# Kernel optimization log

Measured on AMD Instinct MI355X. Metric: run time of the kernel, lower is better.

Reference implementation:

```python
import jax, jax.numpy as jnp
import numpy as np

H = 8          # SD1.4 heads
TAU = 0.1      # HarmCfg.tau
GAMMA = 1.0    # HarmCfg.gamma
EPS = 1e-12    # F.normalize eps


def setup_inputs() -> dict:
    key = jax.random.key(0)
    ks = jax.random.split(key, 8)
    B, S, C, K, D = 16, 4096, 320, 77, 768
    return {
        "hidden_states": jax.random.normal(ks[0], (B, S, C), jnp.float32),
        "encoder_hidden_states": jax.random.normal(ks[1], (B, K, D), jnp.float32),
        "harm_vec": jax.random.normal(ks[2], (D,), jnp.float32),
        "Wq": jax.random.normal(ks[3], (C, C), jnp.float32) * 0.02,
        "Wk": jax.random.normal(ks[4], (D, C), jnp.float32) * 0.02,
        "Wv": jax.random.normal(ks[5], (D, C), jnp.float32) * 0.02,
        "Wo": jax.random.normal(ks[6], (C, C), jnp.float32) * 0.02,
        "bo": jnp.zeros((C,), jnp.float32),
    }


def reference(hidden_states, encoder_hidden_states, harm_vec, Wq, Wk, Wv, Wo, bo):
    B, S, C = hidden_states.shape
    K = encoder_hidden_states.shape[1]
    dh = C // H
    scale = 1.0 / jnp.sqrt(jnp.asarray(dh, hidden_states.dtype))

    # projections (no bias on q/k/v, as in diffusers SD1.4)
    q = (hidden_states @ Wq).reshape(B, S, H, dh)
    k = (encoder_hidden_states @ Wk).reshape(B, K, H, dh)
    v = (encoder_hidden_states @ Wv).reshape(B, K, H, dh)

    # scores: QK^T / sqrt(dh)  -> [B, H, S, K]
    scores = jnp.einsum('bqhd,bkhd->bhqk', q, k) * scale

    # cosine-similarity harmful-token penalty (broadcast over heads and queries)
    harm = harm_vec / jnp.maximum(jnp.linalg.norm(harm_vec), EPS)
    ctx_norm = encoder_hidden_states / jnp.maximum(
        jnp.linalg.norm(encoder_hidden_states, axis=-1, keepdims=True), EPS)
    cos = jnp.einsum('bkd,d->bk', ctx_norm, harm)            # [B, K]
    penalty = jnp.maximum(cos - TAU, 0.0)                     # clamp(min=0)
    scores = scores - GAMMA * penalty[:, None, None, :]

    probs = jax.nn.softmax(scores, axis=-1)                   # dropout p=0 (eval)
    out = jnp.einsum('bhqk,bkhd->bqhd', probs, v).reshape(B, S, C)
    return out @ Wo + bo
```

## Files before the change

### kernel.cpp

```cpp
#include <hip/hip_runtime.h>
#include <hip/hip_bf16.h>

#define B_ 16
#define S_ 4096
#define C_ 320
#define KK_ 77
#define D_ 768
#define H_ 8
#define DH_ 40
#define KP_ 80
#define NP_ (H_ * KP_)
#define TAU_ 0.1f
#define GAMMA_ 1.0f
#define EPS_ 1e-12f

typedef __bf16 bf16x8 __attribute__((ext_vector_type(8)));
typedef float f32x4 __attribute__((ext_vector_type(4)));
typedef unsigned short ushort8v __attribute__((ext_vector_type(8)));
typedef unsigned int u32;

#define WAITV(N)  asm volatile("s_waitcnt vmcnt(" #N ")" ::: "memory")
#define WAITLG()  asm volatile("s_waitcnt lgkmcnt(0)" ::: "memory")
#define BAR()     __builtin_amdgcn_s_barrier()

__device__ __forceinline__ unsigned short f2bf(float f) {
    union { float f; unsigned u; } v; v.f = f;
    unsigned r = v.u + 0x7fffu + ((v.u >> 16) & 1u);
    return (unsigned short)(r >> 16);
}

__device__ __forceinline__ void gld16(const unsigned short* g, char* l) {
    __builtin_amdgcn_global_load_lds(
        (const __attribute__((address_space(1))) u32*)g,
        (__attribute__((address_space(3))) u32*)l, 16, 0, 0);
}

__global__ __launch_bounds__(256) void build_M(const float* __restrict__ Wq,
        const float* __restrict__ Wk, const float* __restrict__ Wv,
        const float* __restrict__ Wo, unsigned short* __restrict__ Bmat) {
    const int Dk = blockIdx.x * 256 + threadIdx.x;
    const int h = blockIdx.y;
    const int which = blockIdx.z >> 2;
    const int c0 = (blockIdx.z & 3) * 80;
    __shared__ float wlds[80 * 44];
    for (int i = threadIdx.x; i < 80 * DH_; i += 256) {
        int c = i / DH_, d = i % DH_;
        wlds[c * 44 + d] = which
            ? Wo[(size_t)(h * DH_ + d) * C_ + (c0 + c)]
            : Wq[(size_t)(c0 + c) * C_ + h * DH_ + d];
    }
    float a[DH_];
    const float* Arow = (which ? Wv : Wk) + (size_t)Dk * C_ + h * DH_;
    #pragma unroll
    for (int d = 0; d < DH_; ++d) a[d] = Arow[d];
    __syncthreads();
    const float scale = 0.15811388300841898f;
    for (int c = 0; c < 80; ++c) {
        float s = 0.f;
        #pragma unroll
        for (int q = 0; q < 10; ++q) {
            float4 wv4 = *(const float4*)&wlds[c * 44 + q * 4];
            s += a[q * 4 + 0] * wv4.x + a[q * 4 + 1] * wv4.y
               + a[q * 4 + 2] * wv4.z + a[q * 4 + 3] * wv4.w;
        }
        if (!which) s *= scale;
        int n = which * 2560 + h * C_ + c0 + c;
        Bmat[(size_t)n * D_ + Dk] = f2bf(s);
    }
}

__global__ __launch_bounds__(256) void prep_ehs(const float* __restrict__ ehs,
        const float* __restrict__ harm, unsigned short* __restrict__ ehs_bf,
        float* __restrict__ pen) {
    const int w = threadIdx.x >> 6, l = threadIdx.x & 63;
    const int kk = blockIdx.x * 4 + w, b = blockIdx.y;
    const size_t obase = ((size_t)b * KP_ + kk) * D_;
    if (kk >= KK_) {
        #pragma unroll
        for (int j = 0; j < 12; ++j) ehs_bf[obase + l + j * 64] = 0;
        if (l == 0) pen[b * KP_ + kk] = 0.f;
        return;
    }
    const float* er = ehs + ((size_t)b * KK_ + kk) * D_;
    float ss = 0.f, dd = 0.f, hh = 0.f;
    #pragma unroll
    for (int j = 0; j < 12; ++j) {
        float e = er[l + j * 64], hv = harm[l + j * 64];
        ehs_bf[obase + l + j * 64] = f2bf(e);
        ss += e * e; dd += e * hv; hh += hv * hv;
    }
    #pragma unroll
    for (int off = 32; off; off >>= 1) {
        ss += __shfl_xor(ss, off);
        dd += __shfl_xor(dd, off);
        hh += __shfl_xor(hh, off);
    }
    if (l == 0) {
        float cs = dd / (fmaxf(sqrtf(ss), EPS_) * fmaxf(sqrtf(hh), EPS_));
        pen[b * KP_ + kk] = GAMMA_ * fmaxf(cs - TAU_, 0.f);
    }
}

__global__ __launch_bounds__(1024) void gemm_WpU(
        const unsigned short* __restrict__ ehs_bf,
        const unsigned short* __restrict__ Bmat,
        unsigned short* __restrict__ Wp, unsigned short* __restrict__ U) {
    const int id = blockIdx.x;
    const int b = id & 15, nt = id >> 4;
    const int tid = threadIdx.x, w = tid >> 6, l = tid & 63;
    const int lrow = l & 15, lgrp = l >> 4, lk = lgrp * 8;
    __shared__ unsigned short Al[80 * 768];
    char* lds = (char*)Al;

    const unsigned short* Ag = ehs_bf + (size_t)b * KP_ * D_;
    #pragma unroll
    for (int it = 0; it < 8; ++it) {
        int ch = tid + it * 1024;
        if (ch < 7680) {
            int byte = ch * 16, row = byte / 1536;
            int a = byte ^ ((row & 7) << 4);
            *(ushort8v*)(lds + a) = *(const ushort8v*)(Ag + ch * 8);
        }
    }
    const int n0 = nt * 512 + w * 32;
    const unsigned short* Br = Bmat + (size_t)(n0 + lrow) * D_ + lk;
    bf16x8 bC[2], bN[2];
    #pragma unroll
    for (int nf = 0; nf < 2; ++nf)
        bC[nf] = *(const bf16x8*)(Br + (size_t)nf * 16 * D_);
    __syncthreads();

    f32x4 acc[5][2];
    #pragma unroll
    for (int mf = 0; mf < 5; ++mf)
        #pragma unroll
        for (int nf = 0; nf < 2; ++nf) acc[mf][nf] = (f32x4){0.f, 0.f, 0.f, 0.f};
    #pragma unroll
    for (int ks = 0; ks < D_ / 32; ++ks) {
        if (ks < D_ / 32 - 1) {
            #pragma unroll
            for (int nf = 0; nf < 2; ++nf)
                bN[nf] = *(const bf16x8*)(Br + (size_t)nf * 16 * D_ + (ks + 1) * 32);
        }
        bf16x8 af[5];
        #pragma unroll
        for (int mf = 0; mf < 5; ++mf) {
            int row = mf * 16 + lrow;
            int a = (row * 1536 + (ks * 32 + lk) * 2) ^ ((row & 7) << 4);
            af[mf] = *(const bf16x8*)(lds + a);
        }
        __builtin_amdgcn_s_setprio(1);
        #pragma unroll
        for (int mf = 0; mf < 5; ++mf)
            #pragma unroll
            for (int nf = 0; nf < 2; ++nf)
                acc[mf][nf] = __builtin_amdgcn_mfma_f32_16x16x32_bf16(
                    af[mf], bC[nf], acc[mf][nf], 0, 0, 0);
        __builtin_amdgcn_s_setprio(0);
        #pragma unroll
        for (int nf = 0; nf < 2; ++nf) bC[nf] = bN[nf];
    }
    #pragma unroll
    for (int nf = 0; nf < 2; ++nf) {
        const int col = n0 + nf * 16 + lrow;
        if (col < 2560) {
            const int h = col / C_, c = col % C_;
            #pragma unroll
            for (int mf = 0; mf < 5; ++mf)
                #pragma unroll
                for (int r = 0; r < 4; ++r) {
                    int kk = mf * 16 + lgrp * 4 + r;
                    Wp[((size_t)b * NP_ + h * KP_ + kk) * C_ + c] = f2bf(acc[mf][nf][r]);
                }
        } else {
            const int n2 = col - 2560;
            const int h = n2 / C_, c = n2 % C_;
            #pragma unroll
            for (int mf = 0; mf < 5; ++mf)
                #pragma unroll
                for (int r = 0; r < 4; ++r) {
                    int kk = mf * 16 + lgrp * 4 + r;
                    U[((size_t)b * C_ + c) * NP_ + h * KP_ + kk] = f2bf(acc[mf][nf][r]);
                }
        }
    }
}

__global__ __launch_bounds__(512, 2) void fused_attn(
        const float* __restrict__ hs, const unsigned short* __restrict__ Wp,
        const unsigned short* __restrict__ U, const float* __restrict__ pen,
        const float* __restrict__ bo, float* __restrict__ out) {
    const int id = blockIdx.x;
    const int xcd = id & 7, rest = id >> 3;
    const int b = xcd * 2 + (rest >> 6);
    const int s0 = (rest & 63) * 64;
    __shared__ __align__(16) char smem[163840];
    char* HS = smem;
    char* PB = smem;
    const int tid = threadIdx.x, w = tid >> 6, l = tid & 63;
    const int lrow = l & 15, lgrp = l >> 4, lk = lgrp * 8;
    const int h = w;
    const int mgrp = w & 1, ngrp = w >> 1;
    char* wbuf = smem + 40960 + w * 3 * 5120;
    char* ubuf = smem + 81920 + w * 2 * 5120;

    const unsigned short* Wpb = Wp + ((size_t)b * NP_ + h * KP_) * C_;
    const unsigned short* Ub  = U  + ((size_t)b * C_ + ngrp * 80) * NP_;

    auto stage_wp = [&](int ks, int slot) {
        char* buf = wbuf + slot * 5120;
        #pragma unroll
        for (int j = 0; j < 5; ++j) {
            int L = j * 64 + l;
            int n = L >> 2, cs = (L & 3) ^ (n & 3);
            gld16(Wpb + (size_t)n * C_ + ks * 32 + cs * 8, buf + j * 1024);
        }
    };
    auto stage_u = [&](int t, int slot) {
        char* buf = ubuf + slot * 5120;
        #pragma unroll
        for (int j = 0; j < 5; ++j) {
            int L = j * 64 + l;
            int c = L >> 2, cs = (L & 3) ^ (c & 3);
            gld16(Ub + (size_t)c * NP_ + t * 32 + cs * 8, buf + j * 1024);
        }
    };

    float4 pv4[5];
    #pragma unroll
    for (int nf = 0; nf < 5; ++nf)
        pv4[nf] = *(const float4*)(pen + b * KP_ + nf * 16 + lgrp * 4);
    const float4* hv = (const float4*)(hs + ((size_t)b * S_ + s0) * C_);
    #pragma unroll
    for (int it = 0; it < 10; ++it) {
        int i = tid + it * 512;
        float4 v = hv[i];
        int r = i / 80, c = (i * 4) % C_;
        ushort4 u;
        u.x = f2bf(v.x); u.y = f2bf(v.y); u.z = f2bf(v.z); u.w = f2bf(v.w);
        int a = (r * 640 + c * 2) ^ ((r & 7) << 4);
        *(ushort4*)(HS + a) = u;
    }
    __syncthreads();
    stage_wp(0, 0);
    stage_wp(1, 1);
    stage_wp(2, 2);

    f32x4 acc[5][4];
    #pragma unroll
    for (int nf = 0; nf < 5; ++nf)
        #pragma unroll
        for (int mf = 0; mf < 4; ++mf) acc[nf][mf] = (f32x4){0.f, 0.f, 0.f, 0.f};
    #pragma unroll
    for (int ks = 0; ks < 10; ++ks) {
        if (ks <= 7)      { WAITV(10); }
        else if (ks == 8) { WAITV(5); }
        else              { WAITV(0); }
        char* rb = wbuf + (ks % 3) * 5120;
        bf16x8 bC[5], hf[4];
        #pragma unroll
        for (int nf = 0; nf < 5; ++nf) {
            int n = nf * 16 + lrow;
            bC[nf] = *(const bf16x8*)(rb + n * 64 + ((lgrp ^ (n & 3)) << 4));
        }
        #pragma unroll
        for (int mf = 0; mf < 4; ++mf) {
            int row = mf * 16 + lrow;
            int a = (row * 640 + (ks * 32 + lk) * 2) ^ ((row & 7) << 4);
            hf[mf] = *(const bf16x8*)(HS + a);
        }
        WAITLG();
        if (ks < 7) stage_wp(ks + 3, ks % 3);
        __builtin_amdgcn_s_setprio(1);
        #pragma unroll
        for (int nf = 0; nf < 5; ++nf)
            #pragma unroll
            for (int mf = 0; mf < 4; ++mf)
                acc[nf][mf] = __builtin_amdgcn_mfma_f32_16x16x32_bf16(
                    bC[nf], hf[mf], acc[nf][mf], 0, 0, 0);
        __builtin_amdgcn_s_setprio(0);
    }

    float inv4[4];
    #pragma unroll
    for (int mf = 0; mf < 4; ++mf) {
        float mx = -1e30f;
        #pragma unroll
        for (int nf = 0; nf < 5; ++nf)
            #pragma unroll
            for (int r = 0; r < 4; ++r) {
                float x = acc[nf][mf][r] - ((const float*)&pv4[nf])[r];
                if (nf == 4 && r >= 1) x = (lgrp == 3) ? -1e30f : x;
                acc[nf][mf][r] = x;
                mx = fmaxf(mx, x);
            }
        mx = fmaxf(mx, __shfl_xor(mx, 16));
        mx = fmaxf(mx, __shfl_xor(mx, 32));
        float s = 0.f;
        #pragma unroll
        for (int nf = 0; nf < 5; ++nf)
            #pragma unroll
            for (int r = 0; r < 4; ++r) {
                float e = __expf(acc[nf][mf][r] - mx);
                acc[nf][mf][r] = e; s += e;
            }
        s += __shfl_xor(s, 16);
        s += __shfl_xor(s, 32);
        inv4[mf] = 1.f / s;
    }

    BAR();

    #pragma unroll
    for (int mf = 0; mf < 4; ++mf) {
        const int m = mf * 16 + lrow;
        const float inv = inv4[mf];
        #pragma unroll
        for (int nf = 0; nf < 5; ++nf) {
            ushort4 u;
            u.x = f2bf(acc[nf][mf][0] * inv);
            u.y = f2bf(acc[nf][mf][1] * inv);
            u.z = f2bf(acc[nf][mf][2] * inv);
            u.w = f2bf(acc[nf][mf][3] * inv);
            int a = (m * 1280 + (h * KP_ + nf * 16 + lgrp * 4) * 2) ^ ((m & 7) << 4);
            *(ushort4*)(PB + a) = u;
        }
    }
    stage_u(0, 0);
    stage_u(1, 1);
    WAITLG();
    BAR();

    f32x4 acc2[5][2];
    #pragma unroll
    for (int nf = 0; nf < 5; ++nf)
        #pragma unroll
        for (int mf = 0; mf < 2; ++mf) acc2[nf][mf] = (f32x4){0.f, 0.f, 0.f, 0.f};
    #pragma unroll
    for (int t = 0; t < 20; ++t) {
        if (t <= 18) { WAITV(5); } else { WAITV(0); }
        char* rb = ubuf + (t & 1) * 5120;
        bf16x8 pa[2], uf[5];
        #pragma unroll
        for (int mf = 0; mf < 2; ++mf) {
            int m = mgrp * 32 + mf * 16 + lrow;
            int a = (m * 1280 + (t * 32 + lk) * 2) ^ ((m & 7) << 4);
            pa[mf] = *(const bf16x8*)(PB + a);
        }
        #pragma unroll
        for (int nf = 0; nf < 5; ++nf) {
            int c = nf * 16 + lrow;
            uf[nf] = *(const bf16x8*)(rb + c * 64 + ((lgrp ^ (c & 3)) << 4));
        }
        WAITLG();
        if (t < 18) stage_u(t + 2, t & 1);
        __builtin_amdgcn_s_setprio(1);
        #pragma unroll
        for (int nf = 0; nf < 5; ++nf)
            #pragma unroll
            for (int mf = 0; mf < 2; ++mf)
                acc2[nf][mf] = __builtin_amdgcn_mfma_f32_16x16x32_bf16(
                    pa[mf], uf[nf], acc2[nf][mf], 0, 0, 0);
        __builtin_amdgcn_s_setprio(0);
    }

    float bov[5];
    #pragma unroll
    for (int nf = 0; nf < 5; ++nf) bov[nf] = bo[ngrp * 80 + nf * 16 + lrow];
    float* op = out + ((size_t)b * S_ + s0) * C_;
    #pragma unroll
    for (int mf = 0; mf < 2; ++mf)
        #pragma unroll
        for (int r = 0; r < 4; ++r)
            #pragma unroll
            for (int nf = 0; nf < 5; ++nf)
                op[(size_t)(mgrp * 32 + mf * 16 + lgrp * 4 + r) * C_ +
                   ngrp * 80 + nf * 16 + lrow] = acc2[nf][mf][r] + bov[nf];
}

extern "C" void kernel_launch(void* const* d_in, const int* in_sizes, int n_in,
                              void* d_out, int out_size, void* d_ws, size_t ws_size,
                              hipStream_t stream) {
    const float* hs   = (const float*)d_in[0];
    const float* ehs  = (const float*)d_in[1];
    const float* harm = (const float*)d_in[2];
    const float* Wq   = (const float*)d_in[3];
    const float* Wk   = (const float*)d_in[4];
    const float* Wv   = (const float*)d_in[5];
    const float* Wo   = (const float*)d_in[6];
    const float* bo   = (const float*)d_in[7];
    float* out = (float*)d_out;

    char* ws = (char*)d_ws;
    unsigned short* ehs_bf = (unsigned short*)(ws);
    unsigned short* Bmat   = (unsigned short*)(ws + 1966080);
    float*          pen    = (float*)        (ws + 9830400);
    unsigned short* Wp     = (unsigned short*)(ws + 9835520);
    unsigned short* U      = (unsigned short*)(ws + 16389120);

    build_M <<<dim3(3, 8, 8),  256, 0, stream>>>(Wq, Wk, Wv, Wo, Bmat);
    prep_ehs<<<dim3(20, 16),   256, 0, stream>>>(ehs, harm, ehs_bf, pen);
    gemm_WpU<<<dim3(160),     1024, 0, stream>>>(ehs_bf, Bmat, Wp, U);
    fused_attn<<<dim3(1024),   512, 0, stream>>>(hs, Wp, U, pen, bo, out);
}
```

Measured before the change: 167.0 us.

## Share LDS staging across waves with 64-wide k-steps and block barriers

Replaces per-wave private triple- and double-buffered staging of Wp and U tiles with one block-wide shared buffer that all waves fill cooperatively. Each k-step is doubled to 64, so there are fewer pipeline iterations, and the buffers use an 8-way XOR swizzle. U prefetch now starts before the softmax so it overlaps with it. The cost is an added block barrier per step and shallower prefetch: Wp is now single-buffered with a full vmcnt(0) wait each step, which can expose global-load latency.

```diff
diff --git a/kernel.cpp b/kernel.cpp
--- a/kernel.cpp
+++ b/kernel.cpp
@@ -20,6 +20,7 @@
 typedef unsigned int u32;
 
 #define WAITV(N)  asm volatile("s_waitcnt vmcnt(" #N ")" ::: "memory")
+#define WAITVL(N) asm volatile("s_waitcnt vmcnt(" #N ") lgkmcnt(0)" ::: "memory")
 #define WAITLG()  asm volatile("s_waitcnt lgkmcnt(0)" ::: "memory")
 #define BAR()     __builtin_amdgcn_s_barrier()
 
@@ -196,33 +197,34 @@
     const int s0 = (rest & 63) * 64;
     __shared__ __align__(16) char smem[163840];
     char* HS = smem;
+    char* WB = smem + 40960;
     char* PB = smem;
+    char* U0 = smem + 81920;
+    char* U1 = smem + 122880;
     const int tid = threadIdx.x, w = tid >> 6, l = tid & 63;
     const int lrow = l & 15, lgrp = l >> 4, lk = lgrp * 8;
     const int h = w;
     const int mgrp = w & 1, ngrp = w >> 1;
-    char* wbuf = smem + 40960 + w * 3 * 5120;
-    char* ubuf = smem + 81920 + w * 2 * 5120;
-
-    const unsigned short* Wpb = Wp + ((size_t)b * NP_ + h * KP_) * C_;
-    const unsigned short* Ub  = U  + ((size_t)b * C_ + ngrp * 80) * NP_;
-
-    auto stage_wp = [&](int ks, int slot) {
-        char* buf = wbuf + slot * 5120;
+
+    const unsigned short* Wpb = Wp + ((size_t)b * NP_) * C_;
+    const unsigned short* Ub  = U  + ((size_t)b * C_) * NP_;
+
+    auto stage_wp = [&](int s) {
+        #pragma unroll
+        for (int j = 0; j < 10; ++j) {
+            int ch = w * 640 + j * 64 + l;
+            int n = ch >> 3, q = ch & 7;
+            gld16(Wpb + (size_t)n * C_ + s * 64 + ((q ^ (n & 7)) << 3),
+                  WB + ch * 16);
+        }
+    };
+    auto stage_u = [&](int t, char* buf) {
         #pragma unroll
         for (int j = 0; j < 5; ++j) {
-            int L = j * 64 + l;
-            int n = L >> 2, cs = (L & 3) ^ (n & 3);
-            gld16(Wpb + (size_t)n * C_ + ks * 32 + cs * 8, buf + j * 1024);
-        }
-    };
-    auto stage_u = [&](int t, int slot) {
-        char* buf = ubuf + slot * 5120;
-        #pragma unroll
-        for (int j = 0; j < 5; ++j) {
-            int L = j * 64 + l;
-            int c = L >> 2, cs = (L & 3) ^ (c & 3);
-            gld16(Ub + (size_t)c * NP_ + t * 32 + cs * 8, buf + j * 1024);
+            int ch = w * 320 + j * 64 + l;
+            int c = ch >> 3, q = ch & 7;
+            gld16(Ub + (size_t)c * NP_ + t * 64 + ((q ^ (c & 7)) << 3),
+                  buf + ch * 16);
         }
     };
 
@@ -242,9 +244,7 @@
         *(ushort4*)(HS + a) = u;
     }
     __syncthreads();
-    stage_wp(0, 0);
-    stage_wp(1, 1);
-    stage_wp(2, 2);
+    stage_wp(0);
 
     f32x4 acc[5][4];
     #pragma unroll
@@ -252,34 +252,45 @@
         #pragma unroll
         for (int mf = 0; mf < 4; ++mf) acc[nf][mf] = (f32x4){0.f, 0.f, 0.f, 0.f};
     #pragma unroll
-    for (int ks = 0; ks < 10; ++ks) {
-        if (ks <= 7)      { WAITV(10); }
-        else if (ks == 8) { WAITV(5); }
-        else              { WAITV(0); }
-        char* rb = wbuf + (ks % 3) * 5120;
-        bf16x8 bC[5], hf[4];
+    for (int s = 0; s < 5; ++s) {
+        WAITV(0);
+        BAR();
+        bf16x8 bC[5][2], hf[4][2];
         #pragma unroll
         for (int nf = 0; nf < 5; ++nf) {
-            int n = nf * 16 + lrow;
-            bC[nf] = *(const bf16x8*)(rb + n * 64 + ((lgrp ^ (n & 3)) << 4));
+            int n = h * KP_ + nf * 16 + lrow;
+            #pragma unroll
+            for (int ss = 0; ss < 2; ++ss)
+                bC[nf][ss] = *(const bf16x8*)(WB + n * 128 +
+                    ((ss * 64 + lgrp * 16) ^ ((n & 7) << 4)));
         }
         #pragma unroll
         for (int mf = 0; mf < 4; ++mf) {
             int row = mf * 16 + lrow;
-            int a = (row * 640 + (ks * 32 + lk) * 2) ^ ((row & 7) << 4);
-            hf[mf] = *(const bf16x8*)(HS + a);
+            #pragma unroll
+            for (int ss = 0; ss < 2; ++ss) {
+                int ks32 = 2 * s + ss;
+                int a = (row * 640 + (ks32 * 32 + lk) * 2) ^ ((row & 7) << 4);
+                hf[mf][ss] = *(const bf16x8*)(HS + a);
+            }
         }
         WAITLG();
-        if (ks < 7) stage_wp(ks + 3, ks % 3);
+        BAR();
+        if (s < 4) stage_wp(s + 1);
         __builtin_amdgcn_s_setprio(1);
         #pragma unroll
-        for (int nf = 0; nf < 5; ++nf)
-            #pragma unroll
-            for (int mf = 0; mf < 4; ++mf)
-                acc[nf][mf] = __builtin_amdgcn_mfma_f32_16x16x32_bf16(
-                    bC[nf], hf[mf], acc[nf][mf], 0, 0, 0);
+        for (int ss = 0; ss < 2; ++ss)
+            #pragma unroll
+            for (int nf = 0; nf < 5; ++nf)
+                #pragma unroll
+                for (int mf = 0; mf < 4; ++mf)
+                    acc[nf][mf] = __builtin_amdgcn_mfma_f32_16x16x32_bf16(
+                        bC[nf][ss], hf[mf][ss], acc[nf][mf], 0, 0, 0);
         __builtin_amdgcn_s_setprio(0);
     }
+
+    stage_u(0, U0);
+    stage_u(1, U1);
 
     float inv4[4];
     #pragma unroll
@@ -309,8 +320,6 @@
         inv4[mf] = 1.f / s;
     }
 
-    BAR();
-
     #pragma unroll
     for (int mf = 0; mf < 4; ++mf) {
         const int m = mf * 16 + lrow;
@@ -326,9 +335,7 @@
             *(ushort4*)(PB + a) = u;
         }
     }
-    stage_u(0, 0);
-    stage_u(1, 1);
-    WAITLG();
+    WAITVL(5);
     BAR();
 
     f32x4 acc2[5][2];
@@ -337,36 +344,48 @@
         #pragma unroll
         for (int mf = 0; mf < 2; ++mf) acc2[nf][mf] = (f32x4){0.f, 0.f, 0.f, 0.f};
     #pragma unroll
-    for (int t = 0; t < 20; ++t) {
-        if (t <= 18) { WAITV(5); } else { WAITV(0); }
-        char* rb = ubuf + (t & 1) * 5120;
-        bf16x8 pa[2], uf[5];
+    for (int t = 0; t < 10; ++t) {
+        if (t > 0) {
+            if (t < 9) { WAITV(5); } else { WAITV(0); }
+            BAR();
+        }
+        char* ub = (t & 1) ? U1 : U0;
+        bf16x8 pa[2][2], uf[5][2];
         #pragma unroll
         for (int mf = 0; mf < 2; ++mf) {
             int m = mgrp * 32 + mf * 16 + lrow;
-            int a = (m * 1280 + (t * 32 + lk) * 2) ^ ((m & 7) << 4);
-            pa[mf] = *(const bf16x8*)(PB + a);
+            #pragma unroll
+            for (int ss = 0; ss < 2; ++ss) {
+                int a = (m * 1280 + (t * 128 + ss * 64 + lgrp * 16)) ^ ((m & 7) << 4);
+                pa[mf][ss] = *(const bf16x8*)(PB + a);
+            }
         }
         #pragma unroll
         for (int nf = 0; nf < 5; ++nf) {
-            int c = nf * 16 + lrow;
-            uf[nf] = *(const bf16x8*)(rb + c * 64 + ((lgrp ^ (c & 3)) << 4));
+            int c = ngrp * KP_ + nf * 16 + lrow;
+            #pragma unroll
+            for (int ss = 0; ss < 2; ++ss)
+                uf[nf][ss] = *(const bf16x8*)(ub + c * 128 +
+                    ((ss * 64 + lgrp * 16) ^ ((c & 7) << 4)));
         }
         WAITLG();
-        if (t < 18) stage_u(t + 2, t & 1);
+        BAR();
+        if (t < 8) stage_u(t + 2, ub);
         __builtin_amdgcn_s_setprio(1);
         #pragma unroll
-        for (int nf = 0; nf < 5; ++nf)
-            #pragma unroll
-            for (int mf = 0; mf < 2; ++mf)
-                acc2[nf][mf] = __builtin_amdgcn_mfma_f32_16x16x32_bf16(
-                    pa[mf], uf[nf], acc2[nf][mf], 0, 0, 0);
+        for (int ss = 0; ss < 2; ++ss)
+            #pragma unroll
+            for (int nf = 0; nf < 5; ++nf)
+                #pragma unroll
+                for (int mf = 0; mf < 2; ++mf)
+                    acc2[nf][mf] = __builtin_amdgcn_mfma_f32_16x16x32_bf16(
+                        pa[mf][ss], uf[nf][ss], acc2[nf][mf], 0, 0, 0);
         __builtin_amdgcn_s_setprio(0);
     }
 
     float bov[5];
     #pragma unroll
-    for (int nf = 0; nf < 5; ++nf) bov[nf] = bo[ngrp * 80 + nf * 16 + lrow];
+    for (int nf = 0; nf < 5; ++nf) bov[nf] = bo[ngrp * KP_ + nf * 16 + lrow];
     float* op = out + ((size_t)b * S_ + s0) * C_;
     #pragma unroll
     for (int mf = 0; mf < 2; ++mf)
@@ -375,7 +394,7 @@
             #pragma unroll
             for (int nf = 0; nf < 5; ++nf)
                 op[(size_t)(mgrp * 32 + mf * 16 + lgrp * 4 + r) * C_ +
-                   ngrp * 80 + nf * 16 + lrow] = acc2[nf][mf][r] + bov[nf];
+                   ngrp * KP_ + nf * 16 + lrow] = acc2[nf][mf][r] + bov[nf];
 }
 
 extern "C" void kernel_launch(void* const* d_in, const int* in_sizes, int n_in,
```

Measured after the change: 161.4 us. 3.4% less time.
